# Kernel tuning notes

Measured on AMD Instinct MI355X. Metric: run time of the kernel, lower is better.

Reference implementation:

```python
import jax, jax.numpy as jnp
import numpy as np

B, T, CIN, H, W = 8, 16, 16, 64, 64
HID, K = 64, 3


def _conv(x, w, b):
    # x: [B, C, H, W], w: [O, C, K, K] -> [B, O, H, W], 'same' padding
    y = jax.lax.conv_general_dilated(x, w, window_strides=(1, 1), padding='SAME',
                                     dimension_numbers=('NCHW', 'OIHW', 'NCHW'))
    return y + b[None, :, None, None]


def setup_inputs() -> dict:
    key = jax.random.key(0)
    ks = jax.random.split(key, 9)
    cin_h = CIN + HID
    s_conv = 1.0 / np.sqrt(cin_h * K * K)
    s_lin = 1.0 / np.sqrt(cin_h)
    return {
        'x': jax.random.normal(ks[0], (B, T, CIN, H, W), dtype=jnp.float32),
        'Wf': jax.random.uniform(ks[1], (HID, cin_h, K, K), jnp.float32, -s_conv, s_conv),
        'bf': jax.random.uniform(ks[2], (HID,), jnp.float32, -s_conv, s_conv),
        'Wi': jax.random.uniform(ks[3], (HID, cin_h, K, K), jnp.float32, -s_conv, s_conv),
        'bi': jax.random.uniform(ks[4], (HID,), jnp.float32, -s_conv, s_conv),
        'Wc': jax.random.uniform(ks[5], (HID, cin_h, K, K), jnp.float32, -s_conv, s_conv),
        'bc': jax.random.uniform(ks[6], (HID,), jnp.float32, -s_conv, s_conv),
        'Wo': jax.random.uniform(ks[7], (HID, cin_h), jnp.float32, -s_lin, s_lin),
        'bo': jax.random.uniform(ks[8], (HID,), jnp.float32, -s_lin, s_lin),
    }


def reference(x, Wf, bf, Wi, bi, Wc, bc, Wo, bo):
    # x: [B, T, CIN, H, W]
    b, t, cin, h, w = x.shape
    h0 = jnp.zeros((b, HID, h, w), x.dtype)
    c0 = jnp.zeros((b, HID, h, w), x.dtype)

    def step(carry, xt):
        hs, cs = carry
        xc = jnp.concatenate([xt, hs], axis=1)          # [B, CIN+HID, H, W]
        f = jax.nn.sigmoid(_conv(xc, Wf, bf))
        i = jax.nn.sigmoid(_conv(xc, Wi, bi))
        g = jnp.tanh(_conv(xc, Wc, bc))
        # Linear over channel dim (torch applies it on transpose(1,3))
        o = jax.nn.sigmoid(jnp.einsum('bchw,oc->bohw', xc, Wo) + bo[None, :, None, None])
        cs = cs * f + i * g
        hs = jnp.tanh(cs) * o
        return (hs, cs), None

    xs = jnp.swapaxes(x, 0, 1)                          # time-major [T, B, CIN, H, W]
    (hT, cT), _ = jax.lax.scan(step, (h0, c0), xs)
    return hT, cT
```

## Files before the change

### kernel.cpp

```cpp
#include <hip/hip_runtime.h>


#define B_ 8
#define T_ 16
#define CIN_ 16
#define HID_ 64
#define H_ 64
#define W_ 64
#define HW_ (H_*W_)
#define CTOT_ 80
#define XS_ROW 34
#define XS_CH 104
#define XS_SIZE (3*XS_ROW*XS_CH)
#define CSTRIDE_ (B_*HID_*HW_)

typedef __attribute__((ext_vector_type(8))) short short8;
typedef __attribute__((ext_vector_type(4))) float f32x4;

__device__ __forceinline__ unsigned short f2bf(float f){
    unsigned u = __float_as_uint(f);
    u = (u + 0x7FFFu + ((u >> 16) & 1u)) >> 16;
    return (unsigned short)u;
}
__device__ __forceinline__ float sigm_(float v){ return 1.0f/(1.0f + __expf(-v)); }
__device__ __forceinline__ float tanh_(float v){ return 2.0f/(1.0f + __expf(-2.0f*v)) - 1.0f; }

__global__ void prep_wfrag(const float* __restrict__ Wf, const float* __restrict__ Wi,
                           const float* __restrict__ Wc, const float* __restrict__ Wo,
                           const float* __restrict__ bf, const float* __restrict__ bi,
                           const float* __restrict__ bc, const float* __restrict__ bo,
                           unsigned short* __restrict__ Wfrag){
    int idx = blockIdx.x*256 + threadIdx.x;
    int j    = idx & 7;
    int lane = (idx >> 3) & 63;
    int frag = idx >> 9;
    int ng = frag & 15;
    int tc = frag >> 4;
    int cc = tc % 3, tap = tc / 3;
    int n = ng*16 + (lane & 15);
    int g = n >> 6, o = n & 63;
    int c = cc*32 + ((lane >> 4) << 3) + j;
    int ky = tap / 3, kx = tap % 3;
    float v = 0.0f;
    if (c < CTOT_){
        if (g == 0)      v = Wf[((o*CTOT_ + c)*3 + ky)*3 + kx];
        else if (g == 1) v = Wi[((o*CTOT_ + c)*3 + ky)*3 + kx];
        else if (g == 2) v = Wc[((o*CTOT_ + c)*3 + ky)*3 + kx];
        else             v = (tap == 4) ? Wo[o*CTOT_ + c] : 0.0f;
    } else if (c == CTOT_ && tap == 4){
        v = (g==0) ? bf[o] : (g==1) ? bi[o] : (g==2) ? bc[o] : bo[o];
    }
    Wfrag[idx] = f2bf(v);
}

__global__ void prep_xbf(const float* __restrict__ x, unsigned short* __restrict__ xbf){
    int idx = blockIdx.x*256 + threadIdx.x;
    int px = idx & 63;
    int y  = (idx >> 6) & 63;
    int bt = idx >> 12;
    const float* src = x + (size_t)bt*CIN_*HW_ + y*W_ + px;
    unsigned short tmp[16];
    #pragma unroll
    for (int c = 0; c < 16; ++c) tmp[c] = f2bf(src[(size_t)c*HW_]);
    uint4* dst = (uint4*)(xbf + (size_t)idx*16);
    dst[0] = *(uint4*)(tmp);
    dst[1] = *(uint4*)(tmp + 8);
}

__global__ __launch_bounds__(256, 4) void lstm_step(
    const unsigned short* __restrict__ xbf,
    const unsigned short* __restrict__ Wfrag,
    float* __restrict__ cbuf,
    const unsigned short* __restrict__ hin,
    unsigned short* __restrict__ hout,
    float* __restrict__ out,
    int t)
{
    __shared__ __align__(16) unsigned short Xs[XS_SIZE];
    const int id   = blockIdx.x;
    const int xcd  = id & 7;
    const int jj   = id >> 3;
    const int y    = xcd*8 + (jj & 7);
    const int b    = (jj >> 3) & 7;
    const int half = jj >> 6;
    const int x0   = half*32;
    const int tid  = threadIdx.x;
    const int lane = tid & 63;
    const int w    = tid >> 6;
    const int l15  = lane & 15;
    const int q    = lane >> 4;

    uint4 z4; z4.x=z4.y=z4.z=z4.w=0u;
    for (int i = tid; i < XS_SIZE/8; i += 256) ((uint4*)Xs)[i] = z4;
    __syncthreads();

    for (int i = tid; i < 204; i += 256){
        int row = i/68, rem = i - row*68;
        int px = rem >> 1, ch8 = rem & 1;
        int yy = y + row - 1, pxg = x0 + px - 1;
        if (yy >= 0 && yy < H_ && pxg >= 0 && pxg < W_){
            uint4 v = *(const uint4*)(xbf + ((((size_t)(b*T_ + t)*H_ + yy)*W_ + pxg)*16 + ch8*8));
            *(uint4*)(Xs + (row*XS_ROW + px)*XS_CH + ch8*8) = v;
        }
    }
    if (t > 0){
        for (int i = tid; i < 816; i += 256){
            int row = i/272, rem = i - row*272;
            int px = rem >> 3, ch8 = rem & 7;
            int yy = y + row - 1, pxg = x0 + px - 1;
            if (yy >= 0 && yy < H_ && pxg >= 0 && pxg < W_){
                uint4 v = *(const uint4*)(hin + ((((size_t)b*H_ + yy)*W_ + pxg)*HID_ + ch8*8));
                *(uint4*)(Xs + (row*XS_ROW + px)*XS_CH + CIN_ + ch8*8) = v;
            }
        }
    }
    for (int i = tid; i < 3*XS_ROW; i += 256)
        Xs[i*XS_CH + CTOT_] = 0x3F80;
    __syncthreads();

    f32x4 acc[4][2];
    #pragma unroll
    for (int g = 0; g < 4; ++g){ acc[g][0] = (f32x4)0.0f; acc[g][1] = (f32x4)0.0f; }

    short8 aC[2], bC[3], bO;
    {
        const unsigned short* ap = Xs + (size_t)l15*XS_CH + q*8;
        aC[0] = *(const short8*)(ap);
        aC[1] = *(const short8*)(ap + 16*XS_CH);
        const unsigned short* bp = Wfrag + (size_t)w*512 + lane*8;
        #pragma unroll
        for (int g = 0; g < 3; ++g) bC[g] = *(const short8*)(bp + ((size_t)g << 11));
    }
    for (int cc = 0; cc < 3; ++cc){
        #pragma unroll 1
        for (int tap = 0; tap < 9; ++tap){
            int ncc = cc, ntap = tap + 1;
            if (ntap == 9){ ntap = 0; ++ncc; }
            const bool have = (ncc < 3);
            short8 aN[2], bN[3];
            if (have){
                const int nky = ntap/3, nkx = ntap - 3*(ntap/3);
                const unsigned short* ap =
                    Xs + (size_t)(nky*XS_ROW + l15 + nkx)*XS_CH + ncc*32 + q*8;
                aN[0] = *(const short8*)(ap);
                aN[1] = *(const short8*)(ap + 16*XS_CH);
                const unsigned short* bp =
                    Wfrag + ((size_t)((ntap*3 + ncc)*16 + w) << 9) + lane*8;
                #pragma unroll
                for (int g = 0; g < 3; ++g) bN[g] = *(const short8*)(bp + ((size_t)g << 11));
            }
            if (tap == 3)
                bO = *(const short8*)(Wfrag + ((size_t)((4*3 + cc)*16 + 12 + w) << 9) + lane*8);
            if (tap == 4){
                acc[3][0] = __builtin_amdgcn_mfma_f32_16x16x32_bf16(aC[0], bO, acc[3][0], 0,0,0);
                acc[3][1] = __builtin_amdgcn_mfma_f32_16x16x32_bf16(aC[1], bO, acc[3][1], 0,0,0);
            }
            #pragma unroll
            for (int g = 0; g < 3; ++g){
                acc[g][0] = __builtin_amdgcn_mfma_f32_16x16x32_bf16(aC[0], bC[g], acc[g][0], 0,0,0);
                acc[g][1] = __builtin_amdgcn_mfma_f32_16x16x32_bf16(aC[1], bC[g], acc[g][1], 0,0,0);
            }
            if (have){
                aC[0]=aN[0]; aC[1]=aN[1];
                bC[0]=bN[0]; bC[1]=bN[1]; bC[2]=bN[2];
            }
        }
    }

    const int o = w*16 + l15;
    #pragma unroll
    for (int mf = 0; mf < 2; ++mf){
        #pragma unroll
        for (int r = 0; r < 4; ++r){
            const int m = mf*16 + q*4 + r;
            const int pxg = x0 + m;
            const float fv = sigm_(acc[0][mf][r]);
            const float iv = sigm_(acc[1][mf][r]);
            const float gv = tanh_(acc[2][mf][r]);
            const float ov = sigm_(acc[3][mf][r]);
            const size_t cidx = (((size_t)(b*H_ + y)*W_ + pxg)*HID_ + o);
            const float cprev = t ? cbuf[cidx] : 0.0f;
            const float cn = cprev*fv + iv*gv;
            const float hn = tanh_(cn)*ov;
            if (t < T_-1){
                cbuf[cidx] = cn;
                hout[cidx] = f2bf(hn);
            } else {
                const size_t oidx = ((((size_t)(b*HID_ + o))*H_ + y)*W_ + pxg);
                out[oidx] = hn;
                out[CSTRIDE_ + oidx] = cn;
            }
        }
    }
}

extern "C" void kernel_launch(void* const* d_in, const int* in_sizes, int n_in,
                              void* d_out, int out_size, void* d_ws, size_t ws_size,
                              hipStream_t stream){
    const float* x  = (const float*)d_in[0];
    const float* Wf = (const float*)d_in[1];
    const float* bf = (const float*)d_in[2];
    const float* Wi = (const float*)d_in[3];
    const float* bi = (const float*)d_in[4];
    const float* Wc = (const float*)d_in[5];
    const float* bc = (const float*)d_in[6];
    const float* Wo = (const float*)d_in[7];
    const float* bo = (const float*)d_in[8];

    unsigned short* Wfrag = (unsigned short*)d_ws;
    unsigned short* xbf   = (unsigned short*)((char*)d_ws + 442368);
    float*          cbuf  = (float*)((char*)d_ws + 442368 + 16777216);
    unsigned short* hbfA  = (unsigned short*)((char*)d_ws + 442368 + 16777216 + 8388608);
    unsigned short* hbfB  = hbfA + CSTRIDE_;

    prep_wfrag<<<dim3(864), dim3(256), 0, stream>>>(Wf, Wi, Wc, Wo, bf, bi, bc, bo, Wfrag);
    prep_xbf<<<dim3(2048), dim3(256), 0, stream>>>(x, xbf);

    for (int t = 0; t < T_; ++t){
        const unsigned short* hi = (t & 1) ? hbfA : hbfB;
        unsigned short*       ho = (t & 1) ? hbfB : hbfA;
        lstm_step<<<dim3(1024), dim3(256), 0, stream>>>(
            xbf, Wfrag, cbuf, hi, ho, (float*)d_out, t);
    }
}
```

Before: 447.3 us.

## Enlarge LSTM step tile to two full rows with 8-wave blocks

Each block now covers two full image rows (64 pixels each) instead of half of one row, using 512 threads arranged as 2 row-waves by 4 channel-waves, with 4 M-fragments per wave. This raises reuse of the weight fragments per LDS and global load and cuts halo overhead: a 4-row halo for 2 output rows instead of 3 rows for 1, and no column halo loads. The cost is more accumulator registers per wave, a larger LDS footprint, and only 256 blocks per step, which may underfill the GPU's compute units.

```diff
diff --git a/kernel.cpp b/kernel.cpp
--- a/kernel.cpp
+++ b/kernel.cpp
@@ -9,9 +9,9 @@
 #define W_ 64
 #define HW_ (H_*W_)
 #define CTOT_ 80
-#define XS_ROW 34
+#define XS_ROW 66
 #define XS_CH 104
-#define XS_SIZE (3*XS_ROW*XS_CH)
+#define XS_SIZE (4*XS_ROW*XS_CH)
 #define CSTRIDE_ (B_*HID_*HW_)
 
 typedef __attribute__((ext_vector_type(8))) short short8;
@@ -67,7 +67,7 @@
     dst[1] = *(uint4*)(tmp + 8);
 }
 
-__global__ __launch_bounds__(256, 4) void lstm_step(
+__global__ __launch_bounds__(512, 2) void lstm_step(
     const unsigned short* __restrict__ xbf,
     const unsigned short* __restrict__ Wfrag,
     float* __restrict__ cbuf,
@@ -79,55 +79,60 @@
     __shared__ __align__(16) unsigned short Xs[XS_SIZE];
     const int id   = blockIdx.x;
     const int xcd  = id & 7;
-    const int jj   = id >> 3;
-    const int y    = xcd*8 + (jj & 7);
-    const int b    = (jj >> 3) & 7;
-    const int half = jj >> 6;
-    const int x0   = half*32;
+    const int j    = id >> 3;
+    const int b    = j >> 2;
+    const int y0   = xcd*8 + ((j & 3) << 1);
     const int tid  = threadIdx.x;
     const int lane = tid & 63;
-    const int w    = tid >> 6;
+    const int wid  = tid >> 6;
+    const int wm   = wid >> 2;
+    const int wn   = wid & 3;
     const int l15  = lane & 15;
     const int q    = lane >> 4;
 
     uint4 z4; z4.x=z4.y=z4.z=z4.w=0u;
-    for (int i = tid; i < XS_SIZE/8; i += 256) ((uint4*)Xs)[i] = z4;
+    for (int i = tid; i < XS_SIZE/8; i += 512) ((uint4*)Xs)[i] = z4;
     __syncthreads();
 
-    for (int i = tid; i < 204; i += 256){
-        int row = i/68, rem = i - row*68;
+    {
+        int row = tid >> 7, rem = tid & 127;
         int px = rem >> 1, ch8 = rem & 1;
-        int yy = y + row - 1, pxg = x0 + px - 1;
-        if (yy >= 0 && yy < H_ && pxg >= 0 && pxg < W_){
-            uint4 v = *(const uint4*)(xbf + ((((size_t)(b*T_ + t)*H_ + yy)*W_ + pxg)*16 + ch8*8));
-            *(uint4*)(Xs + (row*XS_ROW + px)*XS_CH + ch8*8) = v;
+        int yy = y0 + row - 1;
+        if (yy >= 0 && yy < H_){
+            uint4 v = *(const uint4*)(xbf + ((((size_t)(b*T_ + t)*H_ + yy)*W_ + px)*16 + ch8*8));
+            *(uint4*)(Xs + ((size_t)(row*XS_ROW + px + 1))*XS_CH + ch8*8) = v;
         }
     }
     if (t > 0){
-        for (int i = tid; i < 816; i += 256){
-            int row = i/272, rem = i - row*272;
+        #pragma unroll
+        for (int k = 0; k < 4; ++k){
+            int i = tid + (k << 9);
+            int row = i >> 9, rem = i & 511;
             int px = rem >> 3, ch8 = rem & 7;
-            int yy = y + row - 1, pxg = x0 + px - 1;
-            if (yy >= 0 && yy < H_ && pxg >= 0 && pxg < W_){
-                uint4 v = *(const uint4*)(hin + ((((size_t)b*H_ + yy)*W_ + pxg)*HID_ + ch8*8));
-                *(uint4*)(Xs + (row*XS_ROW + px)*XS_CH + CIN_ + ch8*8) = v;
-            }
-        }
-    }
-    for (int i = tid; i < 3*XS_ROW; i += 256)
+            int yy = y0 + row - 1;
+            if (yy >= 0 && yy < H_){
+                uint4 v = *(const uint4*)(hin + ((((size_t)b*H_ + yy)*W_ + px)*HID_ + ch8*8));
+                *(uint4*)(Xs + (size_t)(row*XS_ROW + px + 1)*XS_CH + CIN_ + ch8*8) = v;
+            }
+        }
+    }
+    for (int i = tid; i < 4*XS_ROW; i += 512)
         Xs[i*XS_CH + CTOT_] = 0x3F80;
     __syncthreads();
 
-    f32x4 acc[4][2];
+    f32x4 acc[4][4];
     #pragma unroll
-    for (int g = 0; g < 4; ++g){ acc[g][0] = (f32x4)0.0f; acc[g][1] = (f32x4)0.0f; }
-
-    short8 aC[2], bC[3], bO;
+    for (int g = 0; g < 4; ++g){
+        #pragma unroll
+        for (int mf = 0; mf < 4; ++mf) acc[g][mf] = (f32x4)0.0f;
+    }
+
+    short8 aC[4], bC[3], bO;
     {
-        const unsigned short* ap = Xs + (size_t)l15*XS_CH + q*8;
-        aC[0] = *(const short8*)(ap);
-        aC[1] = *(const short8*)(ap + 16*XS_CH);
-        const unsigned short* bp = Wfrag + (size_t)w*512 + lane*8;
+        const unsigned short* ap = Xs + (size_t)(wm*XS_ROW + l15)*XS_CH + q*8;
+        #pragma unroll
+        for (int mf = 0; mf < 4; ++mf) aC[mf] = *(const short8*)(ap + mf*16*XS_CH);
+        const unsigned short* bp = Wfrag + (size_t)wn*512 + lane*8;
         #pragma unroll
         for (int g = 0; g < 3; ++g) bC[g] = *(const short8*)(bp + ((size_t)g << 11));
     }
@@ -137,48 +142,51 @@
             int ncc = cc, ntap = tap + 1;
             if (ntap == 9){ ntap = 0; ++ncc; }
             const bool have = (ncc < 3);
-            short8 aN[2], bN[3];
+            short8 aN[4], bN[3];
             if (have){
                 const int nky = ntap/3, nkx = ntap - 3*(ntap/3);
                 const unsigned short* ap =
-                    Xs + (size_t)(nky*XS_ROW + l15 + nkx)*XS_CH + ncc*32 + q*8;
-                aN[0] = *(const short8*)(ap);
-                aN[1] = *(const short8*)(ap + 16*XS_CH);
+                    Xs + (size_t)((wm + nky)*XS_ROW + l15 + nkx)*XS_CH + ncc*32 + q*8;
+                #pragma unroll
+                for (int mf = 0; mf < 4; ++mf) aN[mf] = *(const short8*)(ap + mf*16*XS_CH);
                 const unsigned short* bp =
-                    Wfrag + ((size_t)((ntap*3 + ncc)*16 + w) << 9) + lane*8;
+                    Wfrag + ((size_t)((ntap*3 + ncc)*16 + wn) << 9) + lane*8;
                 #pragma unroll
                 for (int g = 0; g < 3; ++g) bN[g] = *(const short8*)(bp + ((size_t)g << 11));
             }
             if (tap == 3)
-                bO = *(const short8*)(Wfrag + ((size_t)((4*3 + cc)*16 + 12 + w) << 9) + lane*8);
+                bO = *(const short8*)(Wfrag + ((size_t)((4*3 + cc)*16 + 12 + wn) << 9) + lane*8);
             if (tap == 4){
-                acc[3][0] = __builtin_amdgcn_mfma_f32_16x16x32_bf16(aC[0], bO, acc[3][0], 0,0,0);
-                acc[3][1] = __builtin_amdgcn_mfma_f32_16x16x32_bf16(aC[1], bO, acc[3][1], 0,0,0);
+                #pragma unroll
+                for (int mf = 0; mf < 4; ++mf)
+                    acc[3][mf] = __builtin_amdgcn_mfma_f32_16x16x32_bf16(aC[mf], bO, acc[3][mf], 0,0,0);
             }
             #pragma unroll
             for (int g = 0; g < 3; ++g){
-                acc[g][0] = __builtin_amdgcn_mfma_f32_16x16x32_bf16(aC[0], bC[g], acc[g][0], 0,0,0);
-                acc[g][1] = __builtin_amdgcn_mfma_f32_16x16x32_bf16(aC[1], bC[g], acc[g][1], 0,0,0);
+                #pragma unroll
+                for (int mf = 0; mf < 4; ++mf)
+                    acc[g][mf] = __builtin_amdgcn_mfma_f32_16x16x32_bf16(aC[mf], bC[g], acc[g][mf], 0,0,0);
             }
             if (have){
-                aC[0]=aN[0]; aC[1]=aN[1];
+                #pragma unroll
+                for (int mf = 0; mf < 4; ++mf) aC[mf] = aN[mf];
                 bC[0]=bN[0]; bC[1]=bN[1]; bC[2]=bN[2];
             }
         }
     }
 
-    const int o = w*16 + l15;
+    const int o = wn*16 + l15;
+    const int y = y0 + wm;
     #pragma unroll
-    for (int mf = 0; mf < 2; ++mf){
+    for (int mf = 0; mf < 4; ++mf){
         #pragma unroll
         for (int r = 0; r < 4; ++r){
-            const int m = mf*16 + q*4 + r;
-            const int pxg = x0 + m;
+            const int px = mf*16 + q*4 + r;
             const float fv = sigm_(acc[0][mf][r]);
             const float iv = sigm_(acc[1][mf][r]);
             const float gv = tanh_(acc[2][mf][r]);
             const float ov = sigm_(acc[3][mf][r]);
-            const size_t cidx = (((size_t)(b*H_ + y)*W_ + pxg)*HID_ + o);
+            const size_t cidx = (((size_t)(b*H_ + y)*W_ + px)*HID_ + o);
             const float cprev = t ? cbuf[cidx] : 0.0f;
             const float cn = cprev*fv + iv*gv;
             const float hn = tanh_(cn)*ov;
@@ -186,7 +194,7 @@
                 cbuf[cidx] = cn;
                 hout[cidx] = f2bf(hn);
             } else {
-                const size_t oidx = ((((size_t)(b*HID_ + o))*H_ + y)*W_ + pxg);
+                const size_t oidx = ((((size_t)(b*HID_ + o))*H_ + y)*W_ + px);
                 out[oidx] = hn;
                 out[CSTRIDE_ + oidx] = cn;
             }
@@ -219,7 +227,7 @@
     for (int t = 0; t < T_; ++t){
         const unsigned short* hi = (t & 1) ? hbfA : hbfB;
         unsigned short*       ho = (t & 1) ? hbfB : hbfA;
-        lstm_step<<<dim3(1024), dim3(256), 0, stream>>>(
+        lstm_step<<<dim3(256), dim3(512), 0, stream>>>(
             xbf, Wfrag, cbuf, hi, ho, (float*)d_out, t);
     }
 }
```

New measurement: 420.4 us. -6.0%, faster.
